# Kernel tuning notes

Hardware: AMD Instinct MI355X
Metric: run time of the kernel (lower is better)

The kernel has to match this reference:

```python
import jax, jax.numpy as jnp
import numpy as np

B, S, I = 64, 64, 512      # batch, seq_len, input_size (encoder hidden)
C = 512                    # context_size (attention dim)
H = 1024                   # decoder hidden (must equal 2*deep_out_size per source)
D = 512                    # deep_out_size
KY = 32000                 # target vocab
M = 512                    # target embedding dim (Ey rows)


def setup_inputs() -> dict:
    key = jax.random.key(0)
    ks = jax.random.split(key, 16)
    sc = 0.05  # small init to keep tanh/softmax in sane range
    return {
        "input_seq": jax.random.normal(ks[0], (B, S, I), jnp.float32),
        "Ey_t": jax.random.normal(ks[1], (KY, M), jnp.float32) * sc,   # Ey.transpose(0,1)
        "W":  jax.random.normal(ks[2], (H, C), jnp.float32) * sc,
        "U":  jax.random.normal(ks[3], (I, C), jnp.float32) * sc,
        "b":  jax.random.normal(ks[4], (C,), jnp.float32) * sc,
        "v":  jax.random.normal(ks[5], (C,), jnp.float32) * sc,
        "W_ih": jax.random.normal(ks[6], (3 * H, C), jnp.float32) * sc,
        "W_hh": jax.random.normal(ks[7], (3 * H, H), jnp.float32) * sc,
        "b_ih": jax.random.normal(ks[8], (3 * H,), jnp.float32) * sc,
        "b_hh": jax.random.normal(ks[9], (3 * H,), jnp.float32) * sc,
        "U_o": jax.random.normal(ks[10], (H, H), jnp.float32) * sc,   # (2*D, hidden) with H==2*D
        "V_o": jax.random.normal(ks[11], (M, H), jnp.float32) * sc,
        "C_o": jax.random.normal(ks[12], (I, H), jnp.float32) * sc,
        "W_o": jax.random.normal(ks[13], (D, KY), jnp.float32) * sc,
    }


def reference(input_seq, Ey_t, W, U, b, v, W_ih, W_hh, b_ih, b_hh, U_o, V_o, C_o, W_o):
    Bn, Sn, In = input_seq.shape
    Hn = W.shape[0]
    Ky = W_o.shape[1]

    # Precompute U_h once, as in source: (B, S, C)
    U_h = jnp.einsum('bsi,ic->bsc', input_seq, U)

    def gru_cell(x, h):
        # torch.nn.GRUCell semantics, gate order r, z, n
        gi = x @ W_ih.T + b_ih
        gh = h @ W_hh.T + b_hh
        i_r, i_z, i_n = jnp.split(gi, 3, axis=-1)
        h_r, h_z, h_n = jnp.split(gh, 3, axis=-1)
        r = jax.nn.sigmoid(i_r + h_r)
        z = jax.nn.sigmoid(i_z + h_z)
        n = jnp.tanh(i_n + r * h_n)
        return (1.0 - z) * n + z * h

    def step(carry, _):
        s, y = carry
        # Additive (Bahdanau) attention over full encoder sequence
        W_s = s @ W                                       # (B, C)
        e = jnp.tanh(W_s[:, None, :] + U_h + b) @ v       # (B, S)
        alpha = jax.nn.softmax(e, axis=1)                 # softmax over seq dim
        ctx = jnp.einsum('bsi,bs->bi', input_seq, alpha)  # (B, I)
        s_new = gru_cell(ctx, s)                          # (B, H)
        # Deep-output with maxout (pool_size=2)
        t = s_new @ U_o + (y @ Ey_t) @ V_o + ctx @ C_o    # (B, 2*D)
        t = t.reshape(Bn, -1, 2).max(axis=-1)             # (B, D)
        prob = jax.nn.softmax(t @ W_o, axis=-1)           # (B, Ky)
        return (s_new, prob), prob

    s0 = jnp.zeros((Bn, Hn), input_seq.dtype)
    y0 = jnp.zeros((Bn, Ky), input_seq.dtype)
    _, probs = jax.lax.scan(step, (s0, y0), None, length=Sn)
    return probs  # (S, B, Ky)
```

## Files before the change

### kernel.cpp

```cpp
#include <hip/hip_runtime.h>
#include <cstdint>
#include <cstddef>

typedef __bf16 bf16;
typedef __bf16 bf16x8 __attribute__((ext_vector_type(8)));
typedef float f32x4 __attribute__((ext_vector_type(4)));

#define MFMA16(a, b, c) __builtin_amdgcn_mfma_f32_16x16x32_bf16((a), (b), (c), 0, 0, 0)

__device__ __forceinline__ float fast_tanh(float x) {
  x = fminf(fmaxf(x, -15.f), 15.f);
  float e = __expf(2.f * x);
  return (e - 1.f) / (e + 1.f);
}
__device__ __forceinline__ float fast_sigmoid(float x) {
  return 1.f / (1.f + __expf(-x));
}


__global__ void cast_split_kernel(const float* __restrict__ src,
                                  bf16* __restrict__ hi, bf16* __restrict__ lo, int n) {
  int i = blockIdx.x * 256 + threadIdx.x;
  if (i < n) {
    float x = src[i];
    bf16 h = (bf16)x;
    hi[i] = h;
    lo[i] = (bf16)(x - (float)h);
  }
}

__global__ void tc_kernel(const float* __restrict__ src, bf16* __restrict__ hi,
                          bf16* __restrict__ lo, int R, int C) {
  __shared__ float tile[32][33];
  int c0 = blockIdx.x * 32, r0 = blockIdx.y * 32;
  int tx = threadIdx.x & 31, ty = threadIdx.x >> 5;
  for (int i = ty; i < 32; i += 8)
    tile[i][tx] = src[(size_t)(r0 + i) * C + c0 + tx];
  __syncthreads();
  for (int i = ty; i < 32; i += 8) {
    float x = tile[tx][i];
    bf16 h = (bf16)x;
    size_t idx = (size_t)(c0 + i) * R + r0 + tx;
    hi[idx] = h;
    if (lo) lo[idx] = (bf16)(x - (float)h);
  }
}


template <int ATOMIC>
__device__ __forceinline__ void gemm_body(const bf16* __restrict__ A, int lda,
                                          const bf16* __restrict__ BT, int ldb,
                                          float* __restrict__ C, int ldc,
                                          int mb, int nb, int k0, int kSteps) {
  int lane = threadIdx.x & 63, wave = threadIdx.x >> 6;
  int mrow = mb * 64 + wave * 16 + (lane & 15);
  int qk = (lane >> 4) * 8;
  const bf16* ap = A + (size_t)mrow * lda + k0 + qk;
  int ncol = nb * 64 + (lane & 15);
  const bf16* bp[4];
#pragma unroll
  for (int j = 0; j < 4; ++j) bp[j] = BT + (size_t)(ncol + 16 * j) * ldb + k0 + qk;
  f32x4 acc[4];
#pragma unroll
  for (int j = 0; j < 4; ++j) acc[j] = {0.f, 0.f, 0.f, 0.f};
  for (int s = 0; s < kSteps; ++s) {
    bf16x8 a = *(const bf16x8*)ap; ap += 32;
#pragma unroll
    for (int j = 0; j < 4; ++j) {
      bf16x8 b = *(const bf16x8*)bp[j]; bp[j] += 32;
      acc[j] = MFMA16(a, b, acc[j]);
    }
  }
  int row = mb * 64 + wave * 16 + (lane >> 4) * 4;
  int col = nb * 64 + (lane & 15);
#pragma unroll
  for (int j = 0; j < 4; ++j)
#pragma unroll
    for (int i = 0; i < 4; ++i) {
      size_t idx = (size_t)(row + i) * ldc + col + j * 16;
      if (ATOMIC) atomicAdd(&C[idx], acc[j][i]); else C[idx] = acc[j][i];
    }
}

__device__ __forceinline__ void gemm_split_body(const bf16* __restrict__ Ahi,
                                                const bf16* __restrict__ Alo, int lda,
                                                const bf16* __restrict__ Bhi,
                                                const bf16* __restrict__ Blo, int ldb,
                                                float* __restrict__ C, int ldc,
                                                int mb, int nb, int kSteps) {
  int lane = threadIdx.x & 63, wave = threadIdx.x >> 6;
  int mrow = mb * 64 + wave * 16 + (lane & 15);
  int qk = (lane >> 4) * 8;
  const bf16* ah = Ahi + (size_t)mrow * lda + qk;
  const bf16* al = Alo + (size_t)mrow * lda + qk;
  int ncol = nb * 64 + (lane & 15);
  const bf16* bh[4]; const bf16* bl[4];
#pragma unroll
  for (int j = 0; j < 4; ++j) {
    bh[j] = Bhi + (size_t)(ncol + 16 * j) * ldb + qk;
    bl[j] = Blo + (size_t)(ncol + 16 * j) * ldb + qk;
  }
  f32x4 acc[4];
#pragma unroll
  for (int j = 0; j < 4; ++j) acc[j] = {0.f, 0.f, 0.f, 0.f};
  for (int s = 0; s < kSteps; ++s) {
    bf16x8 Ah = *(const bf16x8*)ah; ah += 32;
    bf16x8 Al = *(const bf16x8*)al; al += 32;
#pragma unroll
    for (int j = 0; j < 4; ++j) {
      bf16x8 Bh = *(const bf16x8*)bh[j]; bh[j] += 32;
      bf16x8 Bl = *(const bf16x8*)bl[j]; bl[j] += 32;
      acc[j] = MFMA16(Ah, Bh, acc[j]);
      acc[j] = MFMA16(Ah, Bl, acc[j]);
      acc[j] = MFMA16(Al, Bh, acc[j]);
    }
  }
  int row = mb * 64 + wave * 16 + (lane >> 4) * 4;
  int col = nb * 64 + (lane & 15);
#pragma unroll
  for (int j = 0; j < 4; ++j)
#pragma unroll
    for (int i = 0; i < 4; ++i)
      C[(size_t)(row + i) * ldc + col + j * 16] = acc[j][i];
}

__global__ __launch_bounds__(256) void gemm_kernel(const bf16* __restrict__ A, int lda,
                                                   const bf16* __restrict__ BT, int ldb,
                                                   float* __restrict__ C, int ldc,
                                                   int nbN, int kSteps) {
  gemm_body<0>(A, lda, BT, ldb, C, ldc, blockIdx.x / nbN, blockIdx.x % nbN, 0, kSteps);
}

__global__ __launch_bounds__(256) void gemm_split_kernel(const bf16* __restrict__ Ahi,
                                                         const bf16* __restrict__ Alo, int lda,
                                                         const bf16* __restrict__ Bhi,
                                                         const bf16* __restrict__ Blo, int ldb,
                                                         float* __restrict__ C, int ldc,
                                                         int nbN, int kSteps) {
  gemm_split_body(Ahi, Alo, lda, Bhi, Blo, ldb, C, ldc, blockIdx.x / nbN, blockIdx.x % nbN, kSteps);
}


__global__ __launch_bounds__(256) void k1_attn_t1(
    const float* __restrict__ Ws, const float* __restrict__ U_h,
    const float* __restrict__ attnb, const float* __restrict__ vvec,
    const float* __restrict__ inseq,
    bf16* __restrict__ ctx_hi, bf16* __restrict__ ctx_lo,
    const bf16* __restrict__ y_bf, const bf16* __restrict__ EyT,
    float* __restrict__ t1f) {
  int bx = blockIdx.x;
  if (bx < 64) {
    __shared__ float sWs[512];
    __shared__ float sV[512];
    __shared__ float sE[64];
    __shared__ float sAl[64];
    int t = threadIdx.x;
    for (int c = t; c < 512; c += 256) {
      sWs[c] = Ws[bx * 512 + c] + attnb[c];
      sV[c] = vvec[c];
    }
    __syncthreads();
    int j = t >> 2, q = t & 3;
    const float* uh = U_h + ((size_t)(bx * 64 + j)) * 512 + q * 128;
    float part = 0.f;
#pragma unroll 4
    for (int c = 0; c < 128; ++c) {
      int cc = q * 128 + c;
      part += sV[cc] * fast_tanh(sWs[cc] + uh[c]);
    }
    part += __shfl_xor(part, 1);
    part += __shfl_xor(part, 2);
    if (q == 0) sE[j] = part;
    __syncthreads();
    if (t < 64) {
      float x = sE[t];
      float m = x;
      for (int off = 32; off; off >>= 1) m = fmaxf(m, __shfl_xor(m, off));
      float a = __expf(x - m);
      float ssum = a;
      for (int off = 32; off; off >>= 1) ssum += __shfl_xor(ssum, off);
      sAl[t] = a / ssum;
    }
    __syncthreads();
    for (int c = t; c < 512; c += 256) {
      float acc = 0.f;
      const float* ip = inseq + ((size_t)bx * 64) * 512 + c;
#pragma unroll 8
      for (int jj = 0; jj < 64; ++jj) acc += sAl[jj] * ip[(size_t)jj * 512];
      bf16 h = (bf16)acc;
      ctx_hi[bx * 512 + c] = h;
      ctx_lo[bx * 512 + c] = (bf16)(acc - (float)h);
    }
  } else {
    int b2 = bx - 64;
    int nb = b2 & 7;
    int kb = b2 >> 3;
    gemm_body<1>(y_bf, 32000, EyT, 32000, t1f, 512, 0, nb, kb * 1280, 40);
  }
}

__global__ __launch_bounds__(256) void k2_gru(
    const bf16* __restrict__ ctx_hi, const bf16* __restrict__ ctx_lo,
    const bf16* __restrict__ s_hi, const bf16* __restrict__ s_lo,
    const bf16* __restrict__ Wih_hi, const bf16* __restrict__ Wih_lo,
    const bf16* __restrict__ Whh_hi, const bf16* __restrict__ Whh_lo,
    const float* __restrict__ b_ih, const float* __restrict__ b_hh,
    const float* __restrict__ s_cur, float* __restrict__ s_next,
    bf16* __restrict__ sn_hi, bf16* __restrict__ sn_lo) {
  int h0 = blockIdx.x * 16;
  int lane = threadIdx.x & 63, wave = threadIdx.x >> 6;
  int m = wave * 16 + (lane & 15);
  int qk = (lane >> 4) * 8;
  int hl = lane & 15;
  f32x4 gi[3], gh[3];
#pragma unroll
  for (int g = 0; g < 3; ++g) { gi[g] = {0.f, 0.f, 0.f, 0.f}; gh[g] = {0.f, 0.f, 0.f, 0.f}; }
  {
    const bf16* ah = ctx_hi + (size_t)m * 512 + qk;
    const bf16* al = ctx_lo + (size_t)m * 512 + qk;
    const bf16* bh[3]; const bf16* bl[3];
#pragma unroll
    for (int g = 0; g < 3; ++g) {
      size_t r = (size_t)(g * 1024 + h0 + hl) * 512 + qk;
      bh[g] = Wih_hi + r; bl[g] = Wih_lo + r;
    }
    for (int s = 0; s < 16; ++s) {
      bf16x8 Ah = *(const bf16x8*)ah; ah += 32;
      bf16x8 Al = *(const bf16x8*)al; al += 32;
#pragma unroll
      for (int g = 0; g < 3; ++g) {
        bf16x8 Bh = *(const bf16x8*)bh[g]; bh[g] += 32;
        bf16x8 Bl = *(const bf16x8*)bl[g]; bl[g] += 32;
        gi[g] = MFMA16(Ah, Bh, gi[g]);
        gi[g] = MFMA16(Ah, Bl, gi[g]);
        gi[g] = MFMA16(Al, Bh, gi[g]);
      }
    }
  }
  {
    const bf16* ah = s_hi + (size_t)m * 1024 + qk;
    const bf16* al = s_lo + (size_t)m * 1024 + qk;
    const bf16* bh[3]; const bf16* bl[3];
#pragma unroll
    for (int g = 0; g < 3; ++g) {
      size_t r = (size_t)(g * 1024 + h0 + hl) * 1024 + qk;
      bh[g] = Whh_hi + r; bl[g] = Whh_lo + r;
    }
    for (int s = 0; s < 32; ++s) {
      bf16x8 Ah = *(const bf16x8*)ah; ah += 32;
      bf16x8 Al = *(const bf16x8*)al; al += 32;
#pragma unroll
      for (int g = 0; g < 3; ++g) {
        bf16x8 Bh = *(const bf16x8*)bh[g]; bh[g] += 32;
        bf16x8 Bl = *(const bf16x8*)bl[g]; bl[g] += 32;
        gh[g] = MFMA16(Ah, Bh, gh[g]);
        gh[g] = MFMA16(Ah, Bl, gh[g]);
        gh[g] = MFMA16(Al, Bh, gh[g]);
      }
    }
  }
  int hg = h0 + hl;
  float bir = b_ih[hg], biz = b_ih[1024 + hg], bin = b_ih[2048 + hg];
  float bhr = b_hh[hg], bhz = b_hh[1024 + hg], bhn = b_hh[2048 + hg];
  int brow0 = wave * 16 + (lane >> 4) * 4;
#pragma unroll
  for (int i = 0; i < 4; ++i) {
    int b = brow0 + i;
    float r = fast_sigmoid(gi[0][i] + bir + gh[0][i] + bhr);
    float z = fast_sigmoid(gi[1][i] + biz + gh[1][i] + bhz);
    float n = fast_tanh(gi[2][i] + bin + r * (gh[2][i] + bhn));
    float so = s_cur[(size_t)b * 1024 + hg];
    float sn = (1.f - z) * n + z * so;
    s_next[(size_t)b * 1024 + hg] = sn;
    bf16 hh = (bf16)sn;
    sn_hi[(size_t)b * 1024 + hg] = hh;
    sn_lo[(size_t)b * 1024 + hg] = (bf16)(sn - (float)hh);
  }
}

__global__ __launch_bounds__(256) void k3_deepout(
    const bf16* __restrict__ sn_hi, const bf16* __restrict__ sn_lo,
    const float* __restrict__ t1f,
    const bf16* __restrict__ ctx_hi, const bf16* __restrict__ ctx_lo,
    const bf16* __restrict__ UoT_hi, const bf16* __restrict__ UoT_lo,
    const bf16* __restrict__ VoT_hi, const bf16* __restrict__ VoT_lo,
    const bf16* __restrict__ CoT_hi, const bf16* __restrict__ CoT_lo,
    const bf16* __restrict__ WT_hi, const bf16* __restrict__ WT_lo,
    bf16* __restrict__ tm_bf, float* __restrict__ Ws_out) {
  int bx = blockIdx.x;
  int lane = threadIdx.x & 63, wave = threadIdx.x >> 6;
  int qk = (lane >> 4) * 8;
  if (bx < 64) {
    int n0 = bx * 16;
    int m = wave * 16 + (lane & 15);
    int nr = n0 + (lane & 15);
    f32x4 acc = {0.f, 0.f, 0.f, 0.f};
    {
      const bf16* ah = sn_hi + (size_t)m * 1024 + qk;
      const bf16* al = sn_lo + (size_t)m * 1024 + qk;
      const bf16* bh = UoT_hi + (size_t)nr * 1024 + qk;
      const bf16* bl = UoT_lo + (size_t)nr * 1024 + qk;
      for (int s = 0; s < 32; ++s) {
        bf16x8 Ah = *(const bf16x8*)ah; ah += 32;
        bf16x8 Al = *(const bf16x8*)al; al += 32;
        bf16x8 Bh = *(const bf16x8*)bh; bh += 32;
        bf16x8 Bl = *(const bf16x8*)bl; bl += 32;
        acc = MFMA16(Ah, Bh, acc); acc = MFMA16(Ah, Bl, acc); acc = MFMA16(Al, Bh, acc);
      }
    }
    {
      const float* ap = t1f + (size_t)m * 512 + qk;
      const bf16* bh = VoT_hi + (size_t)nr * 512 + qk;
      const bf16* bl = VoT_lo + (size_t)nr * 512 + qk;
      for (int s = 0; s < 16; ++s) {
        f32x4 f0 = *(const f32x4*)ap;
        f32x4 f1 = *(const f32x4*)(ap + 4);
        ap += 32;
        bf16x8 Ah, Al;
#pragma unroll
        for (int i = 0; i < 4; ++i) {
          bf16 h = (bf16)f0[i]; Ah[i] = h; Al[i] = (bf16)(f0[i] - (float)h);
          h = (bf16)f1[i]; Ah[4 + i] = h; Al[4 + i] = (bf16)(f1[i] - (float)h);
        }
        bf16x8 Bh = *(const bf16x8*)bh; bh += 32;
        bf16x8 Bl = *(const bf16x8*)bl; bl += 32;
        acc = MFMA16(Ah, Bh, acc); acc = MFMA16(Ah, Bl, acc); acc = MFMA16(Al, Bh, acc);
      }
    }
    {
      const bf16* ah = ctx_hi + (size_t)m * 512 + qk;
      const bf16* al = ctx_lo + (size_t)m * 512 + qk;
      const bf16* bh = CoT_hi + (size_t)nr * 512 + qk;
      const bf16* bl = CoT_lo + (size_t)nr * 512 + qk;
      for (int s = 0; s < 16; ++s) {
        bf16x8 Ah = *(const bf16x8*)ah; ah += 32;
        bf16x8 Al = *(const bf16x8*)al; al += 32;
        bf16x8 Bh = *(const bf16x8*)bh; bh += 32;
        bf16x8 Bl = *(const bf16x8*)bl; bl += 32;
        acc = MFMA16(Ah, Bh, acc); acc = MFMA16(Ah, Bl, acc); acc = MFMA16(Al, Bh, acc);
      }
    }
    int col = lane & 15;
    int row0 = wave * 16 + (lane >> 4) * 4;
#pragma unroll
    for (int i = 0; i < 4; ++i) {
      float vme = acc[i];
      float vot = __shfl_xor(vme, 1);
      float mx = fmaxf(vme, vot);
      if (!(col & 1)) {
        int d = (n0 + col) >> 1;
        tm_bf[(size_t)(row0 + i) * 512 + d] = (bf16)mx;
      }
    }
  } else {
    gemm_split_body(sn_hi, sn_lo, 1024, WT_hi, WT_lo, 1024, Ws_out, 512, 0, bx - 64, 32);
  }
}

__global__ __launch_bounds__(1024) void k5_softmax(
    const float* __restrict__ logits, float* __restrict__ out,
    bf16* __restrict__ y_bf, float* __restrict__ t1f, int step) {
  int b = blockIdx.x, t = threadIdx.x;
  const float* lr = logits + (size_t)b * 32000;
  float x[32];
  float mx = -1e30f;
#pragma unroll
  for (int i = 0; i < 32; ++i) {
    int k = i * 1024 + t;
    if (k < 32000) { float v = lr[k]; x[i] = v; mx = fmaxf(mx, v); }
  }
  __shared__ float red[16];
  int lane = t & 63, wv = t >> 6;
  for (int off = 32; off; off >>= 1) mx = fmaxf(mx, __shfl_xor(mx, off));
  if (lane == 0) red[wv] = mx;
  __syncthreads();
  if (wv == 0) {
    float m2 = (lane < 16) ? red[lane] : -1e30f;
    for (int off = 8; off; off >>= 1) m2 = fmaxf(m2, __shfl_xor(m2, off));
    if (lane == 0) red[0] = m2;
  }
  __syncthreads();
  mx = red[0];
  __syncthreads();
  float sum = 0.f;
#pragma unroll
  for (int i = 0; i < 32; ++i) {
    int k = i * 1024 + t;
    if (k < 32000) { float e = __expf(x[i] - mx); x[i] = e; sum += e; }
  }
  for (int off = 32; off; off >>= 1) sum += __shfl_xor(sum, off);
  if (lane == 0) red[wv] = sum;
  __syncthreads();
  if (wv == 0) {
    float s2 = (lane < 16) ? red[lane] : 0.f;
    for (int off = 8; off; off >>= 1) s2 += __shfl_xor(s2, off);
    if (lane == 0) red[0] = s2;
  }
  __syncthreads();
  float inv = 1.f / red[0];
  float* orow = out + ((size_t)step * 64 + b) * 32000;
  bf16* yrow = y_bf + (size_t)b * 32000;
#pragma unroll
  for (int i = 0; i < 32; ++i) {
    int k = i * 1024 + t;
    if (k < 32000) {
      float p = x[i] * inv;
      orow[k] = p;
      yrow[k] = (bf16)p;
    }
  }
  if (t < 512) t1f[(size_t)b * 512 + t] = 0.f;
}


extern "C" void kernel_launch(void* const* d_in, const int* in_sizes, int n_in,
                              void* d_out, int out_size, void* d_ws, size_t ws_size,
                              hipStream_t stream) {
  const float* input_seq = (const float*)d_in[0];
  const float* Ey_t = (const float*)d_in[1];
  const float* W = (const float*)d_in[2];
  const float* U = (const float*)d_in[3];
  const float* attnb = (const float*)d_in[4];
  const float* vvec = (const float*)d_in[5];
  const float* W_ih = (const float*)d_in[6];
  const float* W_hh = (const float*)d_in[7];
  const float* b_ih = (const float*)d_in[8];
  const float* b_hh = (const float*)d_in[9];
  const float* U_o = (const float*)d_in[10];
  const float* V_o = (const float*)d_in[11];
  const float* C_o = (const float*)d_in[12];
  const float* W_o = (const float*)d_in[13];
  float* out = (float*)d_out;

  char* p = (char*)d_ws;
  auto alloc = [&](size_t bytes) -> char* {
    char* r = p;
    p += (bytes + 255) & ~(size_t)255;
    return r;
  };
  float* sbuf0 = (float*)alloc(64 * 1024 * 4);
  bf16* shi0 = (bf16*)alloc(64 * 1024 * 2);
  bf16* slo0 = (bf16*)alloc(64 * 1024 * 2);
  float* Ws = (float*)alloc(64 * 512 * 4);
  float* t1f = (float*)alloc(64 * 512 * 4);
  bf16* y_bf = (bf16*)alloc((size_t)64 * 32000 * 2);
  size_t zeroBytes = (size_t)(p - (char*)d_ws);
  float* sbuf1 = (float*)alloc(64 * 1024 * 4);
  bf16* shi1 = (bf16*)alloc(64 * 1024 * 2);
  bf16* slo1 = (bf16*)alloc(64 * 1024 * 2);
  bf16* ctx_hi = (bf16*)alloc(64 * 512 * 2);
  bf16* ctx_lo = (bf16*)alloc(64 * 512 * 2);
  bf16* tm_bf = (bf16*)alloc(64 * 512 * 2);
  float* logits = (float*)alloc((size_t)64 * 32000 * 4);
  float* U_h = (float*)alloc((size_t)4096 * 512 * 4);
  bf16* in_hi = (bf16*)alloc((size_t)4096 * 512 * 2);
  bf16* in_lo = (bf16*)alloc((size_t)4096 * 512 * 2);
  bf16* UT_hi = (bf16*)alloc(512 * 512 * 2);
  bf16* UT_lo = (bf16*)alloc(512 * 512 * 2);
  bf16* EyT = (bf16*)alloc((size_t)512 * 32000 * 2);
  bf16* WoT = (bf16*)alloc((size_t)32000 * 512 * 2);
  bf16* UoT_hi = (bf16*)alloc((size_t)1024 * 1024 * 2);
  bf16* UoT_lo = (bf16*)alloc((size_t)1024 * 1024 * 2);
  bf16* VoT_hi = (bf16*)alloc((size_t)1024 * 512 * 2);
  bf16* VoT_lo = (bf16*)alloc((size_t)1024 * 512 * 2);
  bf16* CoT_hi = (bf16*)alloc((size_t)1024 * 512 * 2);
  bf16* CoT_lo = (bf16*)alloc((size_t)1024 * 512 * 2);
  bf16* WT_hi = (bf16*)alloc((size_t)512 * 1024 * 2);
  bf16* WT_lo = (bf16*)alloc((size_t)512 * 1024 * 2);
  bf16* Wih_hi = (bf16*)alloc((size_t)3072 * 512 * 2);
  bf16* Wih_lo = (bf16*)alloc((size_t)3072 * 512 * 2);
  bf16* Whh_hi = (bf16*)alloc((size_t)3072 * 1024 * 2);
  bf16* Whh_lo = (bf16*)alloc((size_t)3072 * 1024 * 2);

  hipMemsetAsync(d_ws, 0, zeroBytes, stream);

  cast_split_kernel<<<(4096 * 512) / 256, 256, 0, stream>>>(input_seq, in_hi, in_lo, 4096 * 512);
  cast_split_kernel<<<(3072 * 512) / 256, 256, 0, stream>>>(W_ih, Wih_hi, Wih_lo, 3072 * 512);
  cast_split_kernel<<<(3072 * 1024) / 256, 256, 0, stream>>>(W_hh, Whh_hi, Whh_lo, 3072 * 1024);
  tc_kernel<<<dim3(512 / 32, 512 / 32), 256, 0, stream>>>(U, UT_hi, UT_lo, 512, 512);
  tc_kernel<<<dim3(512 / 32, 32000 / 32), 256, 0, stream>>>(Ey_t, EyT, nullptr, 32000, 512);
  tc_kernel<<<dim3(32000 / 32, 512 / 32), 256, 0, stream>>>(W_o, WoT, nullptr, 512, 32000);
  tc_kernel<<<dim3(1024 / 32, 1024 / 32), 256, 0, stream>>>(U_o, UoT_hi, UoT_lo, 1024, 1024);
  tc_kernel<<<dim3(1024 / 32, 512 / 32), 256, 0, stream>>>(V_o, VoT_hi, VoT_lo, 512, 1024);
  tc_kernel<<<dim3(1024 / 32, 512 / 32), 256, 0, stream>>>(C_o, CoT_hi, CoT_lo, 512, 1024);
  tc_kernel<<<dim3(512 / 32, 1024 / 32), 256, 0, stream>>>(W, WT_hi, WT_lo, 1024, 512);
  gemm_split_kernel<<<64 * 8, 256, 0, stream>>>(in_hi, in_lo, 512, UT_hi, UT_lo, 512,
                                                U_h, 512, 8, 16);

  float* sb[2] = {sbuf0, sbuf1};
  bf16* sh[2] = {shi0, shi1};
  bf16* sl[2] = {slo0, slo1};

  for (int t = 0; t < 64; ++t) {
    int cur = t & 1;
    k1_attn_t1<<<264, 256, 0, stream>>>(Ws, U_h, attnb, vvec, input_seq,
                                        ctx_hi, ctx_lo, y_bf, EyT, t1f);
    k2_gru<<<64, 256, 0, stream>>>(ctx_hi, ctx_lo, sh[cur], sl[cur],
                                   Wih_hi, Wih_lo, Whh_hi, Whh_lo, b_ih, b_hh,
                                   sb[cur], sb[cur ^ 1], sh[cur ^ 1], sl[cur ^ 1]);
    k3_deepout<<<72, 256, 0, stream>>>(sh[cur ^ 1], sl[cur ^ 1], t1f, ctx_hi, ctx_lo,
                                       UoT_hi, UoT_lo, VoT_hi, VoT_lo, CoT_hi, CoT_lo,
                                       WT_hi, WT_lo, tm_bf, Ws);
    gemm_kernel<<<500, 256, 0, stream>>>(tm_bf, 512, WoT, 512, logits, 32000, 500, 16);
    k5_softmax<<<64, 1024, 0, stream>>>(logits, out, y_bf, t1f, t);
  }
  (void)in_sizes; (void)n_in; (void)out_size; (void)ws_size;
}
```

Measured before the change: 10.25 ms.

## Fuse softmax into logits GEMM with deferred normalization and split-K GRU/deepout

Removes the separate softmax kernel. The logits GEMM now writes exp(logit) and per-block partial sums. Normalization is deferred: the next step's attention kernel writes the output rows scaled by 1/Z, and the deepout kernel folds 1/Z into the y@Ey path while feeding unnormalized bf16 exponentials as y. GRU and deepout kernels move to 1024 threads with split-K over four wave groups and an LDS reduction, and the Ey GEMM gets finer K splitting. The risk is that skipping max subtraction in the exp could overflow for larger logits, and scaling by 1/Z after the bf16 product changes rounding.

```diff
diff --git a/kernel.cpp b/kernel.cpp
--- a/kernel.cpp
+++ b/kernel.cpp
@@ -63,6 +63,7 @@
   f32x4 acc[4];
 #pragma unroll
   for (int j = 0; j < 4; ++j) acc[j] = {0.f, 0.f, 0.f, 0.f};
+#pragma unroll 4
   for (int s = 0; s < kSteps; ++s) {
     bf16x8 a = *(const bf16x8*)ap; ap += 32;
 #pragma unroll
@@ -103,6 +104,7 @@
   f32x4 acc[4];
 #pragma unroll
   for (int j = 0; j < 4; ++j) acc[j] = {0.f, 0.f, 0.f, 0.f};
+#pragma unroll 2
   for (int s = 0; s < kSteps; ++s) {
     bf16x8 Ah = *(const bf16x8*)ah; ah += 32;
     bf16x8 Al = *(const bf16x8*)al; al += 32;
@@ -122,13 +124,6 @@
 #pragma unroll
     for (int i = 0; i < 4; ++i)
       C[(size_t)(row + i) * ldc + col + j * 16] = acc[j][i];
-}
-
-__global__ __launch_bounds__(256) void gemm_kernel(const bf16* __restrict__ A, int lda,
-                                                   const bf16* __restrict__ BT, int ldb,
-                                                   float* __restrict__ C, int ldc,
-                                                   int nbN, int kSteps) {
-  gemm_body<0>(A, lda, BT, ldb, C, ldc, blockIdx.x / nbN, blockIdx.x % nbN, 0, kSteps);
 }
 
 __global__ __launch_bounds__(256) void gemm_split_kernel(const bf16* __restrict__ Ahi,
@@ -147,7 +142,9 @@
     const float* __restrict__ inseq,
     bf16* __restrict__ ctx_hi, bf16* __restrict__ ctx_lo,
     const bf16* __restrict__ y_bf, const bf16* __restrict__ EyT,
-    float* __restrict__ t1f) {
+    float* __restrict__ t1f,
+    const float* __restrict__ Ef, const float* __restrict__ Zpart,
+    float* __restrict__ invZ, float* __restrict__ out, int step) {
   int bx = blockIdx.x;
   if (bx < 64) {
     __shared__ float sWs[512];
@@ -191,15 +188,42 @@
       ctx_hi[bx * 512 + c] = h;
       ctx_lo[bx * 512 + c] = (bf16)(acc - (float)h);
     }
-  } else {
+  } else if (bx < 464) {
     int b2 = bx - 64;
     int nb = b2 & 7;
     int kb = b2 >> 3;
-    gemm_body<1>(y_bf, 32000, EyT, 32000, t1f, 512, 0, nb, kb * 1280, 40);
-  }
-}
-
-__global__ __launch_bounds__(256) void k2_gru(
+    gemm_body<1>(y_bf, 32000, EyT, 32000, t1f, 512, 0, nb, kb * 640, 20);
+  } else {
+    int r = bx - 464;
+    int t = threadIdx.x;
+    float part = 0.f;
+    for (int nb = t; nb < 500; nb += 256) part += Zpart[nb * 64 + r];
+    for (int off = 32; off; off >>= 1) part += __shfl_xor(part, off);
+    __shared__ float w4[4];
+    __shared__ float sIz;
+    if ((t & 63) == 0) w4[t >> 6] = part;
+    __syncthreads();
+    if (t == 0) {
+      float Zs = w4[0] + w4[1] + w4[2] + w4[3];
+      float iz = (step == 0) ? 0.f : 1.f / Zs;
+      invZ[r] = iz;
+      sIz = iz;
+    }
+    __syncthreads();
+    if (step > 0) {
+      float iz = sIz;
+      const f32x4* er = (const f32x4*)(Ef + (size_t)r * 32000);
+      f32x4* orow = (f32x4*)(out + ((size_t)(step - 1) * 64 + r) * 32000);
+      for (int v = t; v < 8000; v += 256) {
+        f32x4 e = er[v];
+        f32x4 o = {e[0] * iz, e[1] * iz, e[2] * iz, e[3] * iz};
+        orow[v] = o;
+      }
+    }
+  }
+}
+
+__global__ __launch_bounds__(1024) void k2_gru(
     const bf16* __restrict__ ctx_hi, const bf16* __restrict__ ctx_lo,
     const bf16* __restrict__ s_hi, const bf16* __restrict__ s_lo,
     const bf16* __restrict__ Wih_hi, const bf16* __restrict__ Wih_lo,
@@ -208,23 +232,26 @@
     const float* __restrict__ s_cur, float* __restrict__ s_next,
     bf16* __restrict__ sn_hi, bf16* __restrict__ sn_lo) {
   int h0 = blockIdx.x * 16;
-  int lane = threadIdx.x & 63, wave = threadIdx.x >> 6;
-  int m = wave * 16 + (lane & 15);
+  int tid = threadIdx.x;
+  int wave = tid >> 6, lane = tid & 63;
+  int rw = wave & 3, kg = wave >> 2;
+  int m = rw * 16 + (lane & 15);
   int qk = (lane >> 4) * 8;
   int hl = lane & 15;
   f32x4 gi[3], gh[3];
 #pragma unroll
   for (int g = 0; g < 3; ++g) { gi[g] = {0.f, 0.f, 0.f, 0.f}; gh[g] = {0.f, 0.f, 0.f, 0.f}; }
   {
-    const bf16* ah = ctx_hi + (size_t)m * 512 + qk;
-    const bf16* al = ctx_lo + (size_t)m * 512 + qk;
+    const bf16* ah = ctx_hi + (size_t)m * 512 + kg * 128 + qk;
+    const bf16* al = ctx_lo + (size_t)m * 512 + kg * 128 + qk;
     const bf16* bh[3]; const bf16* bl[3];
 #pragma unroll
     for (int g = 0; g < 3; ++g) {
-      size_t r = (size_t)(g * 1024 + h0 + hl) * 512 + qk;
+      size_t r = (size_t)(g * 1024 + h0 + hl) * 512 + kg * 128 + qk;
       bh[g] = Wih_hi + r; bl[g] = Wih_lo + r;
     }
-    for (int s = 0; s < 16; ++s) {
+#pragma unroll
+    for (int s = 0; s < 4; ++s) {
       bf16x8 Ah = *(const bf16x8*)ah; ah += 32;
       bf16x8 Al = *(const bf16x8*)al; al += 32;
 #pragma unroll
@@ -238,15 +265,16 @@
     }
   }
   {
-    const bf16* ah = s_hi + (size_t)m * 1024 + qk;
-    const bf16* al = s_lo + (size_t)m * 1024 + qk;
+    const bf16* ah = s_hi + (size_t)m * 1024 + kg * 256 + qk;
+    const bf16* al = s_lo + (size_t)m * 1024 + kg * 256 + qk;
     const bf16* bh[3]; const bf16* bl[3];
 #pragma unroll
     for (int g = 0; g < 3; ++g) {
-      size_t r = (size_t)(g * 1024 + h0 + hl) * 1024 + qk;
+      size_t r = (size_t)(g * 1024 + h0 + hl) * 1024 + kg * 256 + qk;
       bh[g] = Whh_hi + r; bl[g] = Whh_lo + r;
     }
-    for (int s = 0; s < 32; ++s) {
+#pragma unroll
+    for (int s = 0; s < 8; ++s) {
       bf16x8 Ah = *(const bf16x8*)ah; ah += 32;
       bf16x8 Al = *(const bf16x8*)al; al += 32;
 #pragma unroll
@@ -259,26 +287,58 @@
       }
     }
   }
-  int hg = h0 + hl;
-  float bir = b_ih[hg], biz = b_ih[1024 + hg], bin = b_ih[2048 + hg];
-  float bhr = b_hh[hg], bhz = b_hh[1024 + hg], bhn = b_hh[2048 + hg];
-  int brow0 = wave * 16 + (lane >> 4) * 4;
-#pragma unroll
-  for (int i = 0; i < 4; ++i) {
-    int b = brow0 + i;
-    float r = fast_sigmoid(gi[0][i] + bir + gh[0][i] + bhr);
-    float z = fast_sigmoid(gi[1][i] + biz + gh[1][i] + bhz);
-    float n = fast_tanh(gi[2][i] + bin + r * (gh[2][i] + bhn));
-    float so = s_cur[(size_t)b * 1024 + hg];
-    float sn = (1.f - z) * n + z * so;
-    s_next[(size_t)b * 1024 + hg] = sn;
-    bf16 hh = (bf16)sn;
-    sn_hi[(size_t)b * 1024 + hg] = hh;
-    sn_lo[(size_t)b * 1024 + hg] = (bf16)(sn - (float)hh);
-  }
-}
-
-__global__ __launch_bounds__(256) void k3_deepout(
+  __shared__ float red[2][4][64][24];
+  if (kg >= 2) {
+    float* d = &red[kg - 2][rw][lane][0];
+#pragma unroll
+    for (int g = 0; g < 3; ++g)
+#pragma unroll
+      for (int i = 0; i < 4; ++i) { d[g * 4 + i] = gi[g][i]; d[12 + g * 4 + i] = gh[g][i]; }
+  }
+  __syncthreads();
+  if (kg < 2) {
+    const float* d = &red[kg][rw][lane][0];
+#pragma unroll
+    for (int g = 0; g < 3; ++g)
+#pragma unroll
+      for (int i = 0; i < 4; ++i) { gi[g][i] += d[g * 4 + i]; gh[g][i] += d[12 + g * 4 + i]; }
+  }
+  __syncthreads();
+  if (kg == 1) {
+    float* d = &red[0][rw][lane][0];
+#pragma unroll
+    for (int g = 0; g < 3; ++g)
+#pragma unroll
+      for (int i = 0; i < 4; ++i) { d[g * 4 + i] = gi[g][i]; d[12 + g * 4 + i] = gh[g][i]; }
+  }
+  __syncthreads();
+  if (kg == 0) {
+    const float* d = &red[0][rw][lane][0];
+#pragma unroll
+    for (int g = 0; g < 3; ++g)
+#pragma unroll
+      for (int i = 0; i < 4; ++i) { gi[g][i] += d[g * 4 + i]; gh[g][i] += d[12 + g * 4 + i]; }
+    int hg = h0 + hl;
+    float bir = b_ih[hg], biz = b_ih[1024 + hg], bin = b_ih[2048 + hg];
+    float bhr = b_hh[hg], bhz = b_hh[1024 + hg], bhn = b_hh[2048 + hg];
+    int brow0 = rw * 16 + (lane >> 4) * 4;
+#pragma unroll
+    for (int i = 0; i < 4; ++i) {
+      int b = brow0 + i;
+      float r = fast_sigmoid(gi[0][i] + bir + gh[0][i] + bhr);
+      float z = fast_sigmoid(gi[1][i] + biz + gh[1][i] + bhz);
+      float n = fast_tanh(gi[2][i] + bin + r * (gh[2][i] + bhn));
+      float so = s_cur[(size_t)b * 1024 + hg];
+      float sn = (1.f - z) * n + z * so;
+      s_next[(size_t)b * 1024 + hg] = sn;
+      bf16 hh = (bf16)sn;
+      sn_hi[(size_t)b * 1024 + hg] = hh;
+      sn_lo[(size_t)b * 1024 + hg] = (bf16)(sn - (float)hh);
+    }
+  }
+}
+
+__global__ __launch_bounds__(1024) void k3_deepout(
     const bf16* __restrict__ sn_hi, const bf16* __restrict__ sn_lo,
     const float* __restrict__ t1f,
     const bf16* __restrict__ ctx_hi, const bf16* __restrict__ ctx_lo,
@@ -286,52 +346,26 @@
     const bf16* __restrict__ VoT_hi, const bf16* __restrict__ VoT_lo,
     const bf16* __restrict__ CoT_hi, const bf16* __restrict__ CoT_lo,
     const bf16* __restrict__ WT_hi, const bf16* __restrict__ WT_lo,
+    const float* __restrict__ invZ,
     bf16* __restrict__ tm_bf, float* __restrict__ Ws_out) {
   int bx = blockIdx.x;
-  int lane = threadIdx.x & 63, wave = threadIdx.x >> 6;
+  int tid = threadIdx.x;
+  int wave = tid >> 6, lane = tid & 63;
+  int rw = wave & 3, kg = wave >> 2;
   int qk = (lane >> 4) * 8;
+  __shared__ f32x4 redD[12][64];
+  __shared__ f32x4 redW[12][64][4];
   if (bx < 64) {
     int n0 = bx * 16;
-    int m = wave * 16 + (lane & 15);
+    int m = rw * 16 + (lane & 15);
     int nr = n0 + (lane & 15);
     f32x4 acc = {0.f, 0.f, 0.f, 0.f};
-    {
-      const bf16* ah = sn_hi + (size_t)m * 1024 + qk;
-      const bf16* al = sn_lo + (size_t)m * 1024 + qk;
-      const bf16* bh = UoT_hi + (size_t)nr * 1024 + qk;
-      const bf16* bl = UoT_lo + (size_t)nr * 1024 + qk;
-      for (int s = 0; s < 32; ++s) {
-        bf16x8 Ah = *(const bf16x8*)ah; ah += 32;
-        bf16x8 Al = *(const bf16x8*)al; al += 32;
-        bf16x8 Bh = *(const bf16x8*)bh; bh += 32;
-        bf16x8 Bl = *(const bf16x8*)bl; bl += 32;
-        acc = MFMA16(Ah, Bh, acc); acc = MFMA16(Ah, Bl, acc); acc = MFMA16(Al, Bh, acc);
-      }
-    }
-    {
-      const float* ap = t1f + (size_t)m * 512 + qk;
-      const bf16* bh = VoT_hi + (size_t)nr * 512 + qk;
-      const bf16* bl = VoT_lo + (size_t)nr * 512 + qk;
-      for (int s = 0; s < 16; ++s) {
-        f32x4 f0 = *(const f32x4*)ap;
-        f32x4 f1 = *(const f32x4*)(ap + 4);
-        ap += 32;
-        bf16x8 Ah, Al;
-#pragma unroll
-        for (int i = 0; i < 4; ++i) {
-          bf16 h = (bf16)f0[i]; Ah[i] = h; Al[i] = (bf16)(f0[i] - (float)h);
-          h = (bf16)f1[i]; Ah[4 + i] = h; Al[4 + i] = (bf16)(f1[i] - (float)h);
-        }
-        bf16x8 Bh = *(const bf16x8*)bh; bh += 32;
-        bf16x8 Bl = *(const bf16x8*)bl; bl += 32;
-        acc = MFMA16(Ah, Bh, acc); acc = MFMA16(Ah, Bl, acc); acc = MFMA16(Al, Bh, acc);
-      }
-    }
-    {
-      const bf16* ah = ctx_hi + (size_t)m * 512 + qk;
-      const bf16* al = ctx_lo + (size_t)m * 512 + qk;
-      const bf16* bh = CoT_hi + (size_t)nr * 512 + qk;
-      const bf16* bl = CoT_lo + (size_t)nr * 512 + qk;
+    if (kg < 2) {
+      const bf16* ah = sn_hi + (size_t)m * 1024 + kg * 512 + qk;
+      const bf16* al = sn_lo + (size_t)m * 1024 + kg * 512 + qk;
+      const bf16* bh = UoT_hi + (size_t)nr * 1024 + kg * 512 + qk;
+      const bf16* bl = UoT_lo + (size_t)nr * 1024 + kg * 512 + qk;
+#pragma unroll 4
       for (int s = 0; s < 16; ++s) {
         bf16x8 Ah = *(const bf16x8*)ah; ah += 32;
         bf16x8 Al = *(const bf16x8*)al; al += 32;
@@ -339,77 +373,188 @@
         bf16x8 Bl = *(const bf16x8*)bl; bl += 32;
         acc = MFMA16(Ah, Bh, acc); acc = MFMA16(Ah, Bl, acc); acc = MFMA16(Al, Bh, acc);
       }
-    }
-    int col = lane & 15;
-    int row0 = wave * 16 + (lane >> 4) * 4;
+    } else if (kg == 2) {
+      float iz = invZ[m];
+      const float* ap = t1f + (size_t)m * 512 + qk;
+      const bf16* bh = VoT_hi + (size_t)nr * 512 + qk;
+      const bf16* bl = VoT_lo + (size_t)nr * 512 + qk;
+#pragma unroll 4
+      for (int s = 0; s < 16; ++s) {
+        f32x4 f0 = *(const f32x4*)ap;
+        f32x4 f1 = *(const f32x4*)(ap + 4);
+        ap += 32;
+        bf16x8 Ah, Al;
+#pragma unroll
+        for (int i = 0; i < 4; ++i) {
+          float x = f0[i] * iz; bf16 h = (bf16)x; Ah[i] = h; Al[i] = (bf16)(x - (float)h);
+          x = f1[i] * iz; h = (bf16)x; Ah[4 + i] = h; Al[4 + i] = (bf16)(x - (float)h);
+        }
+        bf16x8 Bh = *(const bf16x8*)bh; bh += 32;
+        bf16x8 Bl = *(const bf16x8*)bl; bl += 32;
+        acc = MFMA16(Ah, Bh, acc); acc = MFMA16(Ah, Bl, acc); acc = MFMA16(Al, Bh, acc);
+      }
+    } else {
+      const bf16* ah = ctx_hi + (size_t)m * 512 + qk;
+      const bf16* al = ctx_lo + (size_t)m * 512 + qk;
+      const bf16* bh = CoT_hi + (size_t)nr * 512 + qk;
+      const bf16* bl = CoT_lo + (size_t)nr * 512 + qk;
+#pragma unroll 4
+      for (int s = 0; s < 16; ++s) {
+        bf16x8 Ah = *(const bf16x8*)ah; ah += 32;
+        bf16x8 Al = *(const bf16x8*)al; al += 32;
+        bf16x8 Bh = *(const bf16x8*)bh; bh += 32;
+        bf16x8 Bl = *(const bf16x8*)bl; bl += 32;
+        acc = MFMA16(Ah, Bh, acc); acc = MFMA16(Ah, Bl, acc); acc = MFMA16(Al, Bh, acc);
+      }
+    }
+    if (kg > 0) redD[wave - 4][lane] = acc;
+    __syncthreads();
+    if (kg == 0) {
+#pragma unroll
+      for (int kgp = 1; kgp < 4; ++kgp) {
+        f32x4 o = redD[kgp * 4 + rw - 4][lane];
+        acc = acc + o;
+      }
+      int col = lane & 15;
+      int row0 = rw * 16 + (lane >> 4) * 4;
+#pragma unroll
+      for (int i = 0; i < 4; ++i) {
+        float vme = acc[i];
+        float vot = __shfl_xor(vme, 1);
+        float mx = fmaxf(vme, vot);
+        if (!(col & 1)) {
+          int d = (n0 + col) >> 1;
+          tm_bf[(size_t)(row0 + i) * 512 + d] = (bf16)mx;
+        }
+      }
+    }
+  } else {
+    int nb = bx - 64;
+    int m = rw * 16 + (lane & 15);
+    int ncol = nb * 64 + (lane & 15);
+    const bf16* ah = sn_hi + (size_t)m * 1024 + kg * 256 + qk;
+    const bf16* al = sn_lo + (size_t)m * 1024 + kg * 256 + qk;
+    const bf16* bh[4]; const bf16* bl[4];
+#pragma unroll
+    for (int j = 0; j < 4; ++j) {
+      size_t r = (size_t)(ncol + 16 * j) * 1024 + kg * 256 + qk;
+      bh[j] = WT_hi + r; bl[j] = WT_lo + r;
+    }
+    f32x4 acc[4];
+#pragma unroll
+    for (int j = 0; j < 4; ++j) acc[j] = {0.f, 0.f, 0.f, 0.f};
+#pragma unroll
+    for (int s = 0; s < 8; ++s) {
+      bf16x8 Ah = *(const bf16x8*)ah; ah += 32;
+      bf16x8 Al = *(const bf16x8*)al; al += 32;
+#pragma unroll
+      for (int j = 0; j < 4; ++j) {
+        bf16x8 Bh = *(const bf16x8*)bh[j]; bh[j] += 32;
+        bf16x8 Bl = *(const bf16x8*)bl[j]; bl[j] += 32;
+        acc[j] = MFMA16(Ah, Bh, acc[j]);
+        acc[j] = MFMA16(Ah, Bl, acc[j]);
+        acc[j] = MFMA16(Al, Bh, acc[j]);
+      }
+    }
+    if (kg > 0) {
+#pragma unroll
+      for (int j = 0; j < 4; ++j) redW[(kg - 1) * 4 + rw][lane][j] = acc[j];
+    }
+    __syncthreads();
+    if (kg == 0) {
+#pragma unroll
+      for (int kgp = 1; kgp < 4; ++kgp)
+#pragma unroll
+        for (int j = 0; j < 4; ++j) {
+          f32x4 o = redW[(kgp - 1) * 4 + rw][lane][j];
+          acc[j] = acc[j] + o;
+        }
+      int row = rw * 16 + (lane >> 4) * 4;
+#pragma unroll
+      for (int j = 0; j < 4; ++j)
+#pragma unroll
+        for (int i = 0; i < 4; ++i)
+          Ws_out[(size_t)(row + i) * 512 + nb * 64 + (lane & 15) + j * 16] = acc[j][i];
+    }
+  }
+}
+
+__global__ __launch_bounds__(256) void k4_logits_exp(
+    const bf16* __restrict__ tm_bf, const bf16* __restrict__ WoT,
+    float* __restrict__ Ef, bf16* __restrict__ Ebf,
+    float* __restrict__ Zpart, float* __restrict__ t1f) {
+  int nb = blockIdx.x;
+  if (nb < 64) {
+    int t = threadIdx.x;
+    t1f[nb * 512 + t] = 0.f;
+    t1f[nb * 512 + 256 + t] = 0.f;
+  }
+  int lane = threadIdx.x & 63, wave = threadIdx.x >> 6;
+  int mrow = wave * 16 + (lane & 15);
+  int qk = (lane >> 4) * 8;
+  const bf16* ap = tm_bf + (size_t)mrow * 512 + qk;
+  int ncol = nb * 64 + (lane & 15);
+  const bf16* bp[4];
+#pragma unroll
+  for (int j = 0; j < 4; ++j) bp[j] = WoT + (size_t)(ncol + 16 * j) * 512 + qk;
+  f32x4 acc[4];
+#pragma unroll
+  for (int j = 0; j < 4; ++j) acc[j] = {0.f, 0.f, 0.f, 0.f};
+#pragma unroll 4
+  for (int s = 0; s < 16; ++s) {
+    bf16x8 a = *(const bf16x8*)ap; ap += 32;
+#pragma unroll
+    for (int j = 0; j < 4; ++j) {
+      bf16x8 b = *(const bf16x8*)bp[j]; bp[j] += 32;
+      acc[j] = MFMA16(a, b, acc[j]);
+    }
+  }
+  int row0 = wave * 16 + (lane >> 4) * 4;
+  int col = nb * 64 + (lane & 15);
+  float rs[4] = {0.f, 0.f, 0.f, 0.f};
+#pragma unroll
+  for (int j = 0; j < 4; ++j)
 #pragma unroll
     for (int i = 0; i < 4; ++i) {
-      float vme = acc[i];
-      float vot = __shfl_xor(vme, 1);
-      float mx = fmaxf(vme, vot);
-      if (!(col & 1)) {
-        int d = (n0 + col) >> 1;
-        tm_bf[(size_t)(row0 + i) * 512 + d] = (bf16)mx;
-      }
-    }
-  } else {
-    gemm_split_body(sn_hi, sn_lo, 1024, WT_hi, WT_lo, 1024, Ws_out, 512, 0, bx - 64, 32);
-  }
-}
-
-__global__ __launch_bounds__(1024) void k5_softmax(
-    const float* __restrict__ logits, float* __restrict__ out,
-    bf16* __restrict__ y_bf, float* __restrict__ t1f, int step) {
-  int b = blockIdx.x, t = threadIdx.x;
-  const float* lr = logits + (size_t)b * 32000;
-  float x[32];
-  float mx = -1e30f;
-#pragma unroll
-  for (int i = 0; i < 32; ++i) {
-    int k = i * 1024 + t;
-    if (k < 32000) { float v = lr[k]; x[i] = v; mx = fmaxf(mx, v); }
-  }
-  __shared__ float red[16];
-  int lane = t & 63, wv = t >> 6;
-  for (int off = 32; off; off >>= 1) mx = fmaxf(mx, __shfl_xor(mx, off));
-  if (lane == 0) red[wv] = mx;
+      float e = __expf(acc[j][i]);
+      size_t idx = (size_t)(row0 + i) * 32000 + col + j * 16;
+      Ef[idx] = e;
+      Ebf[idx] = (bf16)e;
+      rs[i] += e;
+    }
+#pragma unroll
+  for (int i = 0; i < 4; ++i) {
+    float s = rs[i];
+    s += __shfl_xor(s, 1); s += __shfl_xor(s, 2); s += __shfl_xor(s, 4); s += __shfl_xor(s, 8);
+    rs[i] = s;
+  }
+  if ((lane & 15) == 0) {
+#pragma unroll
+    for (int i = 0; i < 4; ++i) Zpart[nb * 64 + row0 + i] = rs[i];
+  }
+}
+
+__global__ __launch_bounds__(256) void k_out_final(
+    const float* __restrict__ Ef, const float* __restrict__ Zpart, float* __restrict__ out) {
+  int r = blockIdx.x;
+  int t = threadIdx.x;
+  float part = 0.f;
+  for (int nb = t; nb < 500; nb += 256) part += Zpart[nb * 64 + r];
+  for (int off = 32; off; off >>= 1) part += __shfl_xor(part, off);
+  __shared__ float w4[4];
+  __shared__ float sIz;
+  if ((t & 63) == 0) w4[t >> 6] = part;
   __syncthreads();
-  if (wv == 0) {
-    float m2 = (lane < 16) ? red[lane] : -1e30f;
-    for (int off = 8; off; off >>= 1) m2 = fmaxf(m2, __shfl_xor(m2, off));
-    if (lane == 0) red[0] = m2;
-  }
+  if (t == 0) sIz = 1.f / (w4[0] + w4[1] + w4[2] + w4[3]);
   __syncthreads();
-  mx = red[0];
-  __syncthreads();
-  float sum = 0.f;
-#pragma unroll
-  for (int i = 0; i < 32; ++i) {
-    int k = i * 1024 + t;
-    if (k < 32000) { float e = __expf(x[i] - mx); x[i] = e; sum += e; }
-  }
-  for (int off = 32; off; off >>= 1) sum += __shfl_xor(sum, off);
-  if (lane == 0) red[wv] = sum;
-  __syncthreads();
-  if (wv == 0) {
-    float s2 = (lane < 16) ? red[lane] : 0.f;
-    for (int off = 8; off; off >>= 1) s2 += __shfl_xor(s2, off);
-    if (lane == 0) red[0] = s2;
-  }
-  __syncthreads();
-  float inv = 1.f / red[0];
-  float* orow = out + ((size_t)step * 64 + b) * 32000;
-  bf16* yrow = y_bf + (size_t)b * 32000;
-#pragma unroll
-  for (int i = 0; i < 32; ++i) {
-    int k = i * 1024 + t;
-    if (k < 32000) {
-      float p = x[i] * inv;
-      orow[k] = p;
-      yrow[k] = (bf16)p;
-    }
-  }
-  if (t < 512) t1f[(size_t)b * 512 + t] = 0.f;
+  float iz = sIz;
+  const f32x4* er = (const f32x4*)(Ef + (size_t)r * 32000);
+  f32x4* orow = (f32x4*)(out + ((size_t)63 * 64 + r) * 32000);
+  for (int v = t; v < 8000; v += 256) {
+    f32x4 e = er[v];
+    f32x4 o = {e[0] * iz, e[1] * iz, e[2] * iz, e[3] * iz};
+    orow[v] = o;
+  }
 }
 
 
@@ -451,7 +596,9 @@
   bf16* ctx_hi = (bf16*)alloc(64 * 512 * 2);
   bf16* ctx_lo = (bf16*)alloc(64 * 512 * 2);
   bf16* tm_bf = (bf16*)alloc(64 * 512 * 2);
-  float* logits = (float*)alloc((size_t)64 * 32000 * 4);
+  float* Ef = (float*)alloc((size_t)64 * 32000 * 4);
+  float* Zpart = (float*)alloc((size_t)500 * 64 * 4);
+  float* invZ = (float*)alloc(64 * 4);
   float* U_h = (float*)alloc((size_t)4096 * 512 * 4);
   bf16* in_hi = (bf16*)alloc((size_t)4096 * 512 * 2);
   bf16* in_lo = (bf16*)alloc((size_t)4096 * 512 * 2);
@@ -493,16 +640,17 @@
 
   for (int t = 0; t < 64; ++t) {
     int cur = t & 1;
-    k1_attn_t1<<<264, 256, 0, stream>>>(Ws, U_h, attnb, vvec, input_seq,
-                                        ctx_hi, ctx_lo, y_bf, EyT, t1f);
-    k2_gru<<<64, 256, 0, stream>>>(ctx_hi, ctx_lo, sh[cur], sl[cur],
-                                   Wih_hi, Wih_lo, Whh_hi, Whh_lo, b_ih, b_hh,
-                                   sb[cur], sb[cur ^ 1], sh[cur ^ 1], sl[cur ^ 1]);
-    k3_deepout<<<72, 256, 0, stream>>>(sh[cur ^ 1], sl[cur ^ 1], t1f, ctx_hi, ctx_lo,
-                                       UoT_hi, UoT_lo, VoT_hi, VoT_lo, CoT_hi, CoT_lo,
-                                       WT_hi, WT_lo, tm_bf, Ws);
-    gemm_kernel<<<500, 256, 0, stream>>>(tm_bf, 512, WoT, 512, logits, 32000, 500, 16);
-    k5_softmax<<<64, 1024, 0, stream>>>(logits, out, y_bf, t1f, t);
-  }
+    k1_attn_t1<<<528, 256, 0, stream>>>(Ws, U_h, attnb, vvec, input_seq,
+                                        ctx_hi, ctx_lo, y_bf, EyT, t1f,
+                                        Ef, Zpart, invZ, out, t);
+    k2_gru<<<64, 1024, 0, stream>>>(ctx_hi, ctx_lo, sh[cur], sl[cur],
+                                    Wih_hi, Wih_lo, Whh_hi, Whh_lo, b_ih, b_hh,
+                                    sb[cur], sb[cur ^ 1], sh[cur ^ 1], sl[cur ^ 1]);
+    k3_deepout<<<72, 1024, 0, stream>>>(sh[cur ^ 1], sl[cur ^ 1], t1f, ctx_hi, ctx_lo,
+                                        UoT_hi, UoT_lo, VoT_hi, VoT_lo, CoT_hi, CoT_lo,
+                                        WT_hi, WT_lo, invZ, tm_bf, Ws);
+    k4_logits_exp<<<500, 256, 0, stream>>>(tm_bf, WoT, Ef, y_bf, Zpart, t1f);
+  }
+  k_out_final<<<64, 256, 0, stream>>>(Ef, Zpart, out);
   (void)in_sizes; (void)n_in; (void)out_size; (void)ws_size;
 }
```

Measured after the change: 9.361 ms. 1.09x faster.
